# Kernel tuning notes

Hardware: AMD Instinct MI355X
Metric: run time of the kernel (lower is better)

Reference implementation:

```python
import jax, jax.numpy as jnp
import numpy as np

D_MODEL = 768; N_LAYERS = 4; SOC_WINDOW = 10
D_INNER = 2 * D_MODEL; D_STATE = 16; DT_RANK = D_MODEL // 16; D_CONV = 4
EPS = 1e-5
B, T = 4, 1024


def setup_inputs() -> dict:
    key = jax.random.key(0)
    ks = jax.random.split(key, 10)
    w = lambda k, s, sc=0.02: jax.random.normal(k, s, jnp.float32) * sc
    return {
        "x": jax.random.normal(ks[0], (B, T, 2 + SOC_WINDOW), jnp.float32),
        "inp_w": w(ks[1], (D_MODEL, 2 + SOC_WINDOW)),
        "inp_b": jnp.zeros((D_MODEL,), jnp.float32),
        "in_proj_w": w(ks[2], (N_LAYERS, 2 * D_INNER, D_MODEL)),
        "conv_w": w(ks[3], (N_LAYERS, D_INNER, D_CONV), 0.1),
        "conv_b": jnp.zeros((N_LAYERS, D_INNER), jnp.float32),
        "x_proj_w": w(ks[4], (N_LAYERS, DT_RANK + 2 * D_STATE, D_INNER)),
        "dt_proj_w": w(ks[5], (N_LAYERS, D_INNER, DT_RANK), 0.05),
        "dt_proj_b": w(ks[6], (N_LAYERS, D_INNER), 0.5),
        "A_log": jnp.tile(jnp.log(jnp.arange(1.0, D_STATE + 1.0, dtype=jnp.float32)), (N_LAYERS, D_INNER, 1)),
        "D_skip": jnp.ones((N_LAYERS, D_INNER), jnp.float32),
        "out_proj_w": w(ks[7], (N_LAYERS, D_MODEL, D_INNER)),
        "ln_w": jnp.ones((N_LAYERS, D_MODEL), jnp.float32),
        "norm_w": jnp.ones((D_MODEL,), jnp.float32),
        "head_w": w(ks[8], (1, D_MODEL)),
        "head_b": jnp.zeros((1,), jnp.float32),
    }


def _rmsnorm(x, w):
    return x * jax.lax.rsqrt(jnp.mean(x * x, axis=-1, keepdims=True) + EPS) * w


def _mamba_block(x, in_w, cw, cb, xp_w, dtw, dtb, A_log, Dsk, out_w):
    Bsz = x.shape[0]
    xz = jnp.einsum('btd,ed->bte', x, in_w)            # (B,T,2*D_INNER)
    xx, z = jnp.split(xz, 2, axis=-1)
    # causal depthwise conv1d (pad left d_conv-1, truncate to T)
    xc = jax.lax.conv_general_dilated(
        jnp.swapaxes(xx, 1, 2), cw[:, None, :], (1,), [(D_CONV - 1, 0)],
        feature_group_count=D_INNER, dimension_numbers=('NCH', 'OIH', 'NCH'))
    xx = jax.nn.silu(jnp.swapaxes(xc + cb[None, :, None], 1, 2))  # (B,T,D_INNER)
    dbc = jnp.einsum('btd,ed->bte', xx, xp_w)          # (B,T,dt_rank+2*N)
    delta = jax.nn.softplus(jnp.einsum('btr,dr->btd', dbc[..., :DT_RANK], dtw) + dtb)
    Bm = dbc[..., DT_RANK:DT_RANK + D_STATE]           # (B,T,N)
    Cm = dbc[..., DT_RANK + D_STATE:]                  # (B,T,N)
    A = -jnp.exp(A_log)                                # (D_INNER,N)

    def step(h, inp):
        d_t, x_t, b_t, c_t = inp                       # (B,Din),(B,Din),(B,N),(B,N)
        h = jnp.exp(d_t[..., None] * A) * h + (d_t * x_t)[..., None] * b_t[:, None, :]
        return h, jnp.einsum('bdn,bn->bd', h, c_t)

    h0 = jnp.zeros((Bsz, D_INNER, D_STATE), x.dtype)
    _, ys = jax.lax.scan(step, h0, (jnp.moveaxis(delta, 1, 0), jnp.moveaxis(xx, 1, 0),
                                    jnp.moveaxis(Bm, 1, 0), jnp.moveaxis(Cm, 1, 0)))
    y = jnp.moveaxis(ys, 0, 1) + Dsk * xx
    y = y * jax.nn.silu(z)
    return jnp.einsum('bte,de->btd', y, out_w)


def reference(x, inp_w, inp_b, in_proj_w, conv_w, conv_b, x_proj_w, dt_proj_w, dt_proj_b,
              A_log, D_skip, out_proj_w, ln_w, norm_w, head_w, head_b):
    h = jnp.einsum('btf,df->btd', x, inp_w) + inp_b
    for l in range(N_LAYERS):
        h = h + _mamba_block(_rmsnorm(h, ln_w[l]), in_proj_w[l], conv_w[l], conv_b[l],
                             x_proj_w[l], dt_proj_w[l], dt_proj_b[l], A_log[l],
                             D_skip[l], out_proj_w[l])
    h = _rmsnorm(h, norm_w)
    y = jnp.einsum('btd,od->bto', h, head_w) + head_b
    return y[..., 0]
```

## Files before the change

### kernel.cpp

```cpp
#include <hip/hip_runtime.h>
#include <stdint.h>

#define D_MODEL   768
#define D_INNER   1536
#define D_STATE   16
#define DT_RANK   48
#define NB        4
#define TSEQ      1024
#define NTOK      4096
#define EPS       1e-5f
#define CHUNK     32
#define NCHUNK    32
#define XP_N      128

typedef __bf16 bf16;
typedef __bf16 bf16x8 __attribute__((ext_vector_type(8)));
typedef float  floatx4 __attribute__((ext_vector_type(4)));
typedef float  f32x2   __attribute__((ext_vector_type(2)));

__device__ __forceinline__ float silu_f(float v)     { return v / (1.f + __expf(-v)); }
__device__ __forceinline__ float softplus_f(float v) { return v > 20.f ? v : __logf(1.f + __expf(v)); }

__device__ __forceinline__ void async_ld16(const void* g, void* l) {
  __builtin_amdgcn_global_load_lds((__attribute__((address_space(1))) uint32_t*)g,
                                   (__attribute__((address_space(3))) uint32_t*)l, 16, 0, 0);
}

__global__ __launch_bounds__(256) void prep_k(const float* __restrict__ win, const float* __restrict__ wout,
                                              const float* __restrict__ wxp,
                                              const float* __restrict__ x, const float* __restrict__ inw,
                                              const float* __restrict__ inb,
                                              bf16* __restrict__ bin, bf16* __restrict__ bout,
                                              bf16* __restrict__ bxp, float* __restrict__ h) {
  const int blk = blockIdx.x;
  if (blk < 55296) {
    const int i = blk * 256 + threadIdx.x;
    const int NIN = 4 * 3072 * 768;
    if (i < NIN) bin[i] = (bf16)win[i];
    else         bout[i - NIN] = (bf16)wout[i - NIN];
  } else if (blk < 58368) {
    const int i = (blk - 55296) * 256 + threadIdx.x;
    const int k = i % 1536;
    const int r = (i / 1536) % XP_N;
    const int l = i / (1536 * XP_N);
    bxp[i] = (r < 80) ? (bf16)wxp[((size_t)l * 80 + r) * 1536 + k] : (bf16)0.f;
  } else {
    const int idx = (blk - 58368) * 256 + threadIdx.x;
    const int d = idx % D_MODEL;
    const int t = idx / D_MODEL;
    float acc = inb[d];
    #pragma unroll
    for (int f = 0; f < 12; ++f) acc = fmaf(x[t * 12 + f], inw[d * 12 + f], acc);
    h[idx] = acc;
  }
}

__global__ __launch_bounds__(256) void rmsnorm_k(const float* __restrict__ h, const float* __restrict__ lnw,
                                                 bf16* __restrict__ xn) {
  const int t = blockIdx.x;
  const float* __restrict__ hr = h + (size_t)t * D_MODEL;
  float v[3];
  float ss = 0.f;
  #pragma unroll
  for (int i = 0; i < 3; ++i) { v[i] = hr[threadIdx.x + i * 256]; ss = fmaf(v[i], v[i], ss); }
  #pragma unroll
  for (int o = 32; o > 0; o >>= 1) ss += __shfl_down(ss, o, 64);
  __shared__ float red[4];
  if ((threadIdx.x & 63) == 0) red[threadIdx.x >> 6] = ss;
  __syncthreads();
  const float tot = red[0] + red[1] + red[2] + red[3];
  const float rs = rsqrtf(tot / (float)D_MODEL + EPS);
  #pragma unroll
  for (int i = 0; i < 3; ++i) {
    const int d = threadIdx.x + i * 256;
    xn[(size_t)t * D_MODEL + d] = (bf16)(v[i] * rs * lnw[d]);
  }
}

template <int MODE>
__global__ __launch_bounds__(256) void gemm_bt(const bf16* __restrict__ A, const bf16* __restrict__ B,
                                               void* __restrict__ Cv, const int N, const int K, const int kLen) {
  alignas(16) __shared__ bf16 As[128 * 32];
  alignas(16) __shared__ bf16 Bs[128 * 32];
  const int tid = threadIdx.x;
  const int lane = tid & 63;
  const int wid = tid >> 6;
  const int wm = wid & 1, wn = wid >> 1;
  const int m0 = blockIdx.x * 128, n0 = blockIdx.y * 128;
  const int kOff = blockIdx.z * kLen;

  floatx4 acc[4][4];
  #pragma unroll
  for (int i = 0; i < 4; ++i)
    #pragma unroll
    for (int j = 0; j < 4; ++j) acc[i][j] = (floatx4){0.f, 0.f, 0.f, 0.f};

  const int srow = lane >> 2;
  const int skp  = (lane & 3) * 8;
  const int fr = lane & 15;
  const int fk = (lane >> 4) * 8;

  for (int k0 = 0; k0 < kLen; k0 += 32) {
    __syncthreads();
    #pragma unroll
    for (int i = 0; i < 2; ++i) {
      const int seg = wid * 2 + i;
      const int row = seg * 16 + srow;
      async_ld16(A + (size_t)(m0 + row) * K + kOff + k0 + skp, (char*)As + seg * 1024);
      async_ld16(B + (size_t)(n0 + row) * K + kOff + k0 + skp, (char*)Bs + seg * 1024);
    }
    __syncthreads();
    bf16x8 a[4], b[4];
    #pragma unroll
    for (int t = 0; t < 4; ++t) {
      a[t] = *(const bf16x8*)&As[(wm * 64 + t * 16 + fr) * 32 + fk];
      b[t] = *(const bf16x8*)&Bs[(wn * 64 + t * 16 + fr) * 32 + fk];
    }
    #pragma unroll
    for (int i = 0; i < 4; ++i)
      #pragma unroll
      for (int j = 0; j < 4; ++j)
        acc[i][j] = __builtin_amdgcn_mfma_f32_16x16x32_bf16(a[i], b[j], acc[i][j], 0, 0, 0);
  }

  const int quad = lane >> 4, col = lane & 15;
  #pragma unroll
  for (int i = 0; i < 4; ++i)
    #pragma unroll
    for (int j = 0; j < 4; ++j) {
      const int gm0 = m0 + wm * 64 + i * 16 + quad * 4;
      const int gn  = n0 + wn * 64 + j * 16 + col;
      #pragma unroll
      for (int r = 0; r < 4; ++r) {
        const size_t off = (size_t)(gm0 + r) * N + gn;
        const float v = acc[i][j][r];
        if (MODE == 0)      ((float*)Cv)[off] = v;
        else if (MODE == 1) ((bf16*)Cv)[off] = (bf16)v;
        else                atomicAdd(&((float*)Cv)[off], v);
      }
    }
}

__global__ __launch_bounds__(256) void conv_silu_k(const bf16* __restrict__ xz, const float* __restrict__ cw,
                                                   const float* __restrict__ cb, bf16* __restrict__ xxb,
                                                   float* __restrict__ dbc) {
  if (blockIdx.x < 512) {
    const int z = blockIdx.x * 256 + threadIdx.x;
    ((float4*)dbc)[z] = (float4){0.f, 0.f, 0.f, 0.f};
  }
  const int idx = blockIdx.x * 256 + threadIdx.x;
  const int d = idx % D_INNER;
  const int bt = idx / D_INNER;
  const int t = bt & (TSEQ - 1);
  float acc = cb[d];
  #pragma unroll
  for (int j = 0; j < 4; ++j) {
    const int tt = t - 3 + j;
    if (tt >= 0) acc = fmaf((float)xz[(size_t)(bt - 3 + j) * (2 * D_INNER) + d], cw[d * 4 + j], acc);
  }
  xxb[idx] = (bf16)silu_f(acc);
}

__global__ __launch_bounds__(256) void scan_p1_k(const bf16* __restrict__ xxb, const float* __restrict__ dbc,
                                                 const float* __restrict__ dtw, const float* __restrict__ dtb,
                                                 const float* __restrict__ Alog,
                                                 float* __restrict__ S, float* __restrict__ su,
                                                 float* __restrict__ delta) {
  const int c = blockIdx.x;
  const int d = blockIdx.y * 256 + threadIdx.x;
  const int b = blockIdx.z;
  f32x2 w2[24];
  #pragma unroll
  for (int k = 0; k < 12; ++k) {
    const float4 t4 = *(const float4*)&dtw[(size_t)d * DT_RANK + k * 4];
    w2[2 * k]     = (f32x2){t4.x, t4.y};
    w2[2 * k + 1] = (f32x2){t4.z, t4.w};
  }
  const float bias = dtb[d];
  float A[16];
  bool fast = true;
  #pragma unroll
  for (int n = 0; n < 16; ++n) {
    A[n] = -__expf(Alog[(size_t)d * 16 + n]);
    fast = fast && (__builtin_fabsf(A[n] + (float)(n + 1)) < 1e-3f);
  }
  f32x2 S2[8];
  #pragma unroll
  for (int k = 0; k < 8; ++k) S2[k] = (f32x2){0.f, 0.f};
  float sus = 0.f;
  const int bt0 = b * TSEQ + c * CHUNK;
  if (fast) {
    for (int tt = 0; tt < CHUNK; ++tt) {
      const size_t bt = bt0 + tt;
      const float* __restrict__ db = dbc + bt * XP_N;
      f32x2 acc2 = (f32x2){bias, 0.f};
      #pragma unroll
      for (int k = 0; k < 24; ++k) acc2 += *(const f32x2*)&db[2 * k] * w2[k];
      const float du = softplus_f(acc2.x + acc2.y);
      delta[bt * D_INNER + d] = du;
      sus += du;
      const float xv  = (float)xxb[bt * D_INNER + d];
      const float dux = du * xv;
      const f32x2 dux2 = (f32x2){dux, dux};
      const float r  = __expf(-du);
      const float rr = r * r;
      f32x2 E = (f32x2){r, rr};
      const f32x2 F = (f32x2){rr, rr};
      const f32x2* __restrict__ B2 = (const f32x2*)(db + DT_RANK);
      #pragma unroll
      for (int k = 0; k < 8; ++k) {
        S2[k] = E * S2[k] + dux2 * B2[k];
        E *= F;
      }
    }
  } else {
    for (int tt = 0; tt < CHUNK; ++tt) {
      const size_t bt = bt0 + tt;
      const float* __restrict__ db = dbc + bt * XP_N;
      float dacc = bias;
      #pragma unroll
      for (int k = 0; k < 24; ++k) { dacc = fmaf(db[2*k], w2[k].x, dacc); dacc = fmaf(db[2*k+1], w2[k].y, dacc); }
      const float du = softplus_f(dacc);
      delta[bt * D_INNER + d] = du;
      sus += du;
      const float xv  = (float)xxb[bt * D_INNER + d];
      const float dux = du * xv;
      const float* __restrict__ Bp = db + DT_RANK;
      #pragma unroll
      for (int n = 0; n < 16; ++n) {
        float* sv = (float*)&S2[n >> 1];
        sv[n & 1] = fmaf(__expf(du * A[n]), sv[n & 1], dux * Bp[n]);
      }
    }
  }
  const size_t base = ((size_t)(b * NCHUNK + c) * 16) * D_INNER + d;
  #pragma unroll
  for (int n = 0; n < 16; ++n) S[base + (size_t)n * D_INNER] = ((const float*)&S2[n >> 1])[n & 1];
  su[(size_t)(b * NCHUNK + c) * D_INNER + d] = sus;
}

__global__ __launch_bounds__(256) void scan_fold_k(const float* __restrict__ Alog, const float* __restrict__ su,
                                                   float* __restrict__ S) {
  const int idx = blockIdx.x * 256 + threadIdx.x;
  const int d = idx % D_INNER;
  const int bn = idx / D_INNER;
  const int n = bn & 15;
  const int b = bn >> 4;
  const float A = -__expf(Alog[(size_t)d * 16 + n]);
  float H = 0.f;
  #pragma unroll 4
  for (int c = 0; c < NCHUNK; ++c) {
    const size_t off = ((size_t)((b * NCHUNK + c) * 16 + n)) * D_INNER + d;
    const float Pv = __expf(A * su[(size_t)(b * NCHUNK + c) * D_INNER + d]);
    const float Sv = S[off];
    S[off] = H;
    H = fmaf(Pv, H, Sv);
  }
}

__global__ __launch_bounds__(256) void scan_p3_k(const bf16* __restrict__ xxb, const float* __restrict__ dbc,
                                                 const float* __restrict__ delta, const float* __restrict__ Alog,
                                                 const float* __restrict__ Hin,
                                                 const bf16* __restrict__ xz, const float* __restrict__ Dsk,
                                                 bf16* __restrict__ yg) {
  const int c = blockIdx.x;
  const int d = blockIdx.y * 256 + threadIdx.x;
  const int b = blockIdx.z;
  const size_t hbase = ((size_t)(b * NCHUNK + c) * 16) * D_INNER + d;
  float A[16];
  f32x2 H2[8];
  bool fast = true;
  #pragma unroll
  for (int n = 0; n < 16; ++n) {
    A[n] = -__expf(Alog[(size_t)d * 16 + n]);
    fast = fast && (__builtin_fabsf(A[n] + (float)(n + 1)) < 1e-3f);
    ((float*)&H2[n >> 1])[n & 1] = Hin[hbase + (size_t)n * D_INNER];
  }
  const float dsk = Dsk[d];
  const int bt0 = b * TSEQ + c * CHUNK;
  if (fast) {
    for (int tt = 0; tt < CHUNK; ++tt) {
      const size_t bt = bt0 + tt;
      const float du  = delta[bt * D_INNER + d];
      const float xv  = (float)xxb[bt * D_INNER + d];
      const float dux = du * xv;
      const f32x2 dux2 = (f32x2){dux, dux};
      const float* __restrict__ db = dbc + bt * XP_N;
      const f32x2* __restrict__ B2 = (const f32x2*)(db + DT_RANK);
      const f32x2* __restrict__ C2 = (const f32x2*)(db + DT_RANK + 16);
      const float r  = __expf(-du);
      const float rr = r * r;
      f32x2 E = (f32x2){r, rr};
      const f32x2 F = (f32x2){rr, rr};
      f32x2 y2 = (f32x2){0.f, 0.f};
      #pragma unroll
      for (int k = 0; k < 8; ++k) {
        H2[k] = E * H2[k] + dux2 * B2[k];
        y2 = H2[k] * C2[k] + y2;
        E *= F;
      }
      const float y = y2.x + y2.y;
      const float z = (float)xz[bt * (2 * D_INNER) + D_INNER + d];
      yg[bt * D_INNER + d] = (bf16)((y + dsk * xv) * silu_f(z));
    }
  } else {
    for (int tt = 0; tt < CHUNK; ++tt) {
      const size_t bt = bt0 + tt;
      const float du  = delta[bt * D_INNER + d];
      const float xv  = (float)xxb[bt * D_INNER + d];
      const float dux = du * xv;
      const float* __restrict__ db = dbc + bt * XP_N;
      const float* __restrict__ Bp = db + DT_RANK;
      const float* __restrict__ Cp = db + DT_RANK + 16;
      float y = 0.f;
      #pragma unroll
      for (int n = 0; n < 16; ++n) {
        float* hv = (float*)&H2[n >> 1];
        hv[n & 1] = fmaf(__expf(du * A[n]), hv[n & 1], dux * Bp[n]);
        y = fmaf(hv[n & 1], Cp[n], y);
      }
      const float z = (float)xz[bt * (2 * D_INNER) + D_INNER + d];
      yg[bt * D_INNER + d] = (bf16)((y + dsk * xv) * silu_f(z));
    }
  }
}

__global__ __launch_bounds__(256) void final_k(const float* __restrict__ h, const float* __restrict__ nw,
                                               const float* __restrict__ hw, const float* __restrict__ hb,
                                               float* __restrict__ out) {
  const int t = blockIdx.x;
  const float* __restrict__ hr = h + (size_t)t * D_MODEL;
  float ss = 0.f, dt_ = 0.f;
  #pragma unroll
  for (int i = 0; i < 3; ++i) {
    const int d = threadIdx.x + i * 256;
    const float v = hr[d];
    ss  = fmaf(v, v, ss);
    dt_ = fmaf(v, nw[d] * hw[d], dt_);
  }
  #pragma unroll
  for (int o = 32; o > 0; o >>= 1) { ss += __shfl_down(ss, o, 64); dt_ += __shfl_down(dt_, o, 64); }
  __shared__ float r0[4], r1[4];
  if ((threadIdx.x & 63) == 0) { r0[threadIdx.x >> 6] = ss; r1[threadIdx.x >> 6] = dt_; }
  __syncthreads();
  if (threadIdx.x == 0) {
    const float sst = r0[0] + r0[1] + r0[2] + r0[3];
    const float dtt = r1[0] + r1[1] + r1[2] + r1[3];
    out[t] = dtt * rsqrtf(sst / (float)D_MODEL + EPS) + hb[0];
  }
}

extern "C" void kernel_launch(void* const* d_in, const int* in_sizes, int n_in,
                              void* d_out, int out_size, void* d_ws, size_t ws_size,
                              hipStream_t stream) {
  (void)in_sizes; (void)n_in; (void)out_size; (void)ws_size;
  const float* x     = (const float*)d_in[0];
  const float* inpw  = (const float*)d_in[1];
  const float* inpb  = (const float*)d_in[2];
  const float* inprj = (const float*)d_in[3];
  const float* convw = (const float*)d_in[4];
  const float* convb = (const float*)d_in[5];
  const float* xprjw = (const float*)d_in[6];
  const float* dtw   = (const float*)d_in[7];
  const float* dtb   = (const float*)d_in[8];
  const float* alog  = (const float*)d_in[9];
  const float* dskip = (const float*)d_in[10];
  const float* outw  = (const float*)d_in[11];
  const float* lnw   = (const float*)d_in[12];
  const float* normw = (const float*)d_in[13];
  const float* headw = (const float*)d_in[14];
  const float* headb = (const float*)d_in[15];
  float* out = (float*)d_out;

  char* p = (char*)d_ws;
  auto take = [&](size_t bytes) { char* q = p; p += (bytes + 255) & ~(size_t)255; return q; };
  bf16*  wbin  = (bf16*) take((size_t)4 * 3072 * 768 * 2);
  bf16*  wbout = (bf16*) take((size_t)4 * 768 * 1536 * 2);
  bf16*  wbxp  = (bf16*) take((size_t)4 * XP_N * 1536 * 2);
  float* h     = (float*)take((size_t)NTOK * D_MODEL * 4);
  bf16*  xn    = (bf16*) take((size_t)NTOK * D_MODEL * 2);
  bf16*  xzb   = (bf16*) take((size_t)NTOK * 2 * D_INNER * 2);
  bf16*  xxb   = (bf16*) take((size_t)NTOK * D_INNER * 2);
  float* dbc   = (float*)take((size_t)NTOK * XP_N * 4);
  float* dlt   = (float*)take((size_t)NTOK * D_INNER * 4);
  float* Sb    = (float*)take((size_t)NB * NCHUNK * 16 * D_INNER * 4);
  float* su    = (float*)take((size_t)NB * NCHUNK * D_INNER * 4);
  bf16*  yg    = (bf16*) take((size_t)NTOK * D_INNER * 2);

  prep_k<<<70656, 256, 0, stream>>>(inprj, outw, xprjw, x, inpw, inpb, wbin, wbout, wbxp, h);

  for (int l = 0; l < 4; ++l) {
    rmsnorm_k<<<NTOK, 256, 0, stream>>>(h, lnw + l * D_MODEL, xn);
    gemm_bt<1><<<dim3(32, 24, 1), 256, 0, stream>>>(xn, wbin + (size_t)l * 3072 * 768, xzb, 3072, 768, 768);
    conv_silu_k<<<NTOK * D_INNER / 256, 256, 0, stream>>>(xzb, convw + l * D_INNER * 4, convb + l * D_INNER,
                                                          xxb, dbc);
    gemm_bt<2><<<dim3(32, 1, 8), 256, 0, stream>>>(xxb, wbxp + (size_t)l * XP_N * 1536, dbc, XP_N, 1536, 192);
    scan_p1_k<<<dim3(NCHUNK, 6, NB), 256, 0, stream>>>(xxb, dbc, dtw + (size_t)l * D_INNER * DT_RANK,
                                                       dtb + l * D_INNER, alog + (size_t)l * D_INNER * 16,
                                                       Sb, su, dlt);
    scan_fold_k<<<NB * 16 * D_INNER / 256, 256, 0, stream>>>(alog + (size_t)l * D_INNER * 16, su, Sb);
    scan_p3_k<<<dim3(NCHUNK, 6, NB), 256, 0, stream>>>(xxb, dbc, dlt, alog + (size_t)l * D_INNER * 16,
                                                       Sb, xzb, dskip + l * D_INNER, yg);
    gemm_bt<2><<<dim3(32, 6, 3), 256, 0, stream>>>(yg, wbout + (size_t)l * 768 * 1536, h, 768, 1536, 512);
  }

  final_k<<<NTOK, 256, 0, stream>>>(h, normw, headw, headb, out);
}
```

Measured before the change: 886.2 us.

## Replace LDS-staged GEMM with register-direct double-buffered global loads

The GEMM kernel no longer stages A/B tiles through shared memory with async global-to-LDS loads and two barriers per k-step. Each wave now loads its MFMA fragments straight from global memory into registers, double-buffered so the next k-slice is fetched while the current one is multiplied, and the K length becomes a template constant. This removes LDS traffic and block barriers, but each wave reloads fragments that other waves share, which raises global/L2 traffic and uses uncoalesced 16-byte row-strided loads.

```diff
diff --git a/kernel.cpp b/kernel.cpp
--- a/kernel.cpp
+++ b/kernel.cpp
@@ -20,11 +20,6 @@
 
 __device__ __forceinline__ float silu_f(float v)     { return v / (1.f + __expf(-v)); }
 __device__ __forceinline__ float softplus_f(float v) { return v > 20.f ? v : __logf(1.f + __expf(v)); }
-
-__device__ __forceinline__ void async_ld16(const void* g, void* l) {
-  __builtin_amdgcn_global_load_lds((__attribute__((address_space(1))) uint32_t*)g,
-                                   (__attribute__((address_space(3))) uint32_t*)l, 16, 0, 0);
-}
 
 __global__ __launch_bounds__(256) void prep_k(const float* __restrict__ win, const float* __restrict__ wout,
                                               const float* __restrict__ wxp,
@@ -77,17 +72,20 @@
   }
 }
 
-template <int MODE>
-__global__ __launch_bounds__(256) void gemm_bt(const bf16* __restrict__ A, const bf16* __restrict__ B,
-                                               void* __restrict__ Cv, const int N, const int K, const int kLen) {
-  alignas(16) __shared__ bf16 As[128 * 32];
-  alignas(16) __shared__ bf16 Bs[128 * 32];
+template <int MODE, int KLEN>
+__global__ __launch_bounds__(256) void gemm_rt(const bf16* __restrict__ A, const bf16* __restrict__ B,
+                                               void* __restrict__ Cv, const int N, const int K) {
   const int tid = threadIdx.x;
   const int lane = tid & 63;
   const int wid = tid >> 6;
   const int wm = wid & 1, wn = wid >> 1;
   const int m0 = blockIdx.x * 128, n0 = blockIdx.y * 128;
-  const int kOff = blockIdx.z * kLen;
+  const int kOff = blockIdx.z * KLEN;
+  const int fr = lane & 15;
+  const int fk = (lane >> 4) * 8;
+
+  const bf16* __restrict__ Ap = A + (size_t)(m0 + wm * 64 + fr) * K + kOff + fk;
+  const bf16* __restrict__ Bp = B + (size_t)(n0 + wn * 64 + fr) * K + kOff + fk;
 
   floatx4 acc[4][4];
   #pragma unroll
@@ -95,32 +93,29 @@
     #pragma unroll
     for (int j = 0; j < 4; ++j) acc[i][j] = (floatx4){0.f, 0.f, 0.f, 0.f};
 
-  const int srow = lane >> 2;
-  const int skp  = (lane & 3) * 8;
-  const int fr = lane & 15;
-  const int fk = (lane >> 4) * 8;
-
-  for (int k0 = 0; k0 < kLen; k0 += 32) {
-    __syncthreads();
-    #pragma unroll
-    for (int i = 0; i < 2; ++i) {
-      const int seg = wid * 2 + i;
-      const int row = seg * 16 + srow;
-      async_ld16(A + (size_t)(m0 + row) * K + kOff + k0 + skp, (char*)As + seg * 1024);
-      async_ld16(B + (size_t)(n0 + row) * K + kOff + k0 + skp, (char*)Bs + seg * 1024);
-    }
-    __syncthreads();
-    bf16x8 a[4], b[4];
-    #pragma unroll
-    for (int t = 0; t < 4; ++t) {
-      a[t] = *(const bf16x8*)&As[(wm * 64 + t * 16 + fr) * 32 + fk];
-      b[t] = *(const bf16x8*)&Bs[(wn * 64 + t * 16 + fr) * 32 + fk];
+  bf16x8 a[2][4], b[2][4];
+  #pragma unroll
+  for (int t = 0; t < 4; ++t) {
+    a[0][t] = *(const bf16x8*)(Ap + (size_t)t * 16 * K);
+    b[0][t] = *(const bf16x8*)(Bp + (size_t)t * 16 * K);
+  }
+  constexpr int NK = KLEN / 32;
+  #pragma unroll 2
+  for (int ki = 0; ki < NK; ++ki) {
+    const int cur = ki & 1, nxt = cur ^ 1;
+    if (ki + 1 < NK) {
+      const int ko = (ki + 1) * 32;
+      #pragma unroll
+      for (int t = 0; t < 4; ++t) {
+        a[nxt][t] = *(const bf16x8*)(Ap + (size_t)t * 16 * K + ko);
+        b[nxt][t] = *(const bf16x8*)(Bp + (size_t)t * 16 * K + ko);
+      }
     }
     #pragma unroll
     for (int i = 0; i < 4; ++i)
       #pragma unroll
       for (int j = 0; j < 4; ++j)
-        acc[i][j] = __builtin_amdgcn_mfma_f32_16x16x32_bf16(a[i], b[j], acc[i][j], 0, 0, 0);
+        acc[i][j] = __builtin_amdgcn_mfma_f32_16x16x32_bf16(a[cur][i], b[cur][j], acc[i][j], 0, 0, 0);
   }
 
   const int quad = lane >> 4, col = lane & 15;
@@ -134,9 +129,8 @@
       for (int r = 0; r < 4; ++r) {
         const size_t off = (size_t)(gm0 + r) * N + gn;
         const float v = acc[i][j][r];
-        if (MODE == 0)      ((float*)Cv)[off] = v;
-        else if (MODE == 1) ((bf16*)Cv)[off] = (bf16)v;
-        else                atomicAdd(&((float*)Cv)[off], v);
+        if (MODE == 1) ((bf16*)Cv)[off] = (bf16)v;
+        else           atomicAdd(&((float*)Cv)[off], v);
       }
     }
 }
@@ -391,17 +385,17 @@
 
   for (int l = 0; l < 4; ++l) {
     rmsnorm_k<<<NTOK, 256, 0, stream>>>(h, lnw + l * D_MODEL, xn);
-    gemm_bt<1><<<dim3(32, 24, 1), 256, 0, stream>>>(xn, wbin + (size_t)l * 3072 * 768, xzb, 3072, 768, 768);
+    gemm_rt<1, 768><<<dim3(32, 24, 1), 256, 0, stream>>>(xn, wbin + (size_t)l * 3072 * 768, xzb, 3072, 768);
     conv_silu_k<<<NTOK * D_INNER / 256, 256, 0, stream>>>(xzb, convw + l * D_INNER * 4, convb + l * D_INNER,
                                                           xxb, dbc);
-    gemm_bt<2><<<dim3(32, 1, 8), 256, 0, stream>>>(xxb, wbxp + (size_t)l * XP_N * 1536, dbc, XP_N, 1536, 192);
+    gemm_rt<2, 192><<<dim3(32, 1, 8), 256, 0, stream>>>(xxb, wbxp + (size_t)l * XP_N * 1536, dbc, XP_N, 1536);
     scan_p1_k<<<dim3(NCHUNK, 6, NB), 256, 0, stream>>>(xxb, dbc, dtw + (size_t)l * D_INNER * DT_RANK,
                                                        dtb + l * D_INNER, alog + (size_t)l * D_INNER * 16,
                                                        Sb, su, dlt);
     scan_fold_k<<<NB * 16 * D_INNER / 256, 256, 0, stream>>>(alog + (size_t)l * D_INNER * 16, su, Sb);
     scan_p3_k<<<dim3(NCHUNK, 6, NB), 256, 0, stream>>>(xxb, dbc, dlt, alog + (size_t)l * D_INNER * 16,
                                                        Sb, xzb, dskip + l * D_INNER, yg);
-    gemm_bt<2><<<dim3(32, 6, 3), 256, 0, stream>>>(yg, wbout + (size_t)l * 768 * 1536, h, 768, 1536, 512);
+    gemm_rt<2, 512><<<dim3(32, 6, 3), 256, 0, stream>>>(yg, wbout + (size_t)l * 768 * 1536, h, 768, 1536);
   }
 
   final_k<<<NTOK, 256, 0, stream>>>(h, normw, headw, headb, out);
```

New measurement: 1.156 ms. +30.4%, slower.
